# Performance work log

Hardware: AMD Instinct MI355X
Metric: run time of the kernel (lower is better)

The kernel has to match this reference:

```python
import jax, jax.numpy as jnp
import numpy as np

SEQ, BATCH, IN, HID, OUT = 2048, 128, 256, 512, 256


def setup_inputs() -> dict:
    key = jax.random.key(0)
    ks = jax.random.split(key, 7)
    s_ih = 1.0 / np.sqrt(HID)
    return {
        "x": jax.random.normal(ks[0], (SEQ, BATCH, IN), dtype=jnp.float32),
        "W_ih": jax.random.normal(ks[1], (HID, IN), dtype=jnp.float32) * s_ih,
        "W_hh": jax.random.normal(ks[2], (HID, HID), dtype=jnp.float32) * s_ih,
        "b_ih": jax.random.normal(ks[3], (HID,), dtype=jnp.float32) * s_ih,
        "b_hh": jax.random.normal(ks[4], (HID,), dtype=jnp.float32) * s_ih,
        "W_fc": jax.random.normal(ks[5], (OUT, HID), dtype=jnp.float32) * s_ih,
        "b_fc": jax.random.normal(ks[6], (OUT,), dtype=jnp.float32) * s_ih,
    }


def reference(x, W_ih, W_hh, b_ih, b_hh, W_fc, b_fc):
    # Precompute input projections for all timesteps with one big GEMM:
    # [S, B, I] @ [I, H] -> [S, B, H]
    x_proj = jnp.einsum("sbi,hi->sbh", x, W_ih) + b_ih + b_hh

    def step(h, xp):  # h: [B, H], xp: [B, H]
        h_new = jnp.tanh(xp + h @ W_hh.T)
        return h_new, None

    h0 = jnp.zeros((x.shape[1], W_hh.shape[0]), dtype=x.dtype)
    h_last, _ = jax.lax.scan(step, h0, x_proj)
    # fc on last timestep's hidden state -> [B, OUT]
    return h_last @ W_fc.T + b_fc
```

## Files before the change

kernel.cpp:

```cpp
#include <hip/hip_runtime.h>
#include <stdint.h>

#define SEQ   2048
#define BATCH 128
#define DIN   256
#define DH    512
#define DOUT  256

typedef uint16_t u16;
typedef uint32_t u32;
typedef __attribute__((ext_vector_type(8))) short short8;
typedef __attribute__((ext_vector_type(4))) float f32x4;
typedef __attribute__((ext_vector_type(4))) int i32x4;

#define TWO_LOG2E 2.8853900817779268f

__device__ __forceinline__ u16 f2bf(float f) {
    u32 u = __float_as_uint(f);
    u += 0x7fffu + ((u >> 16) & 1u);
    return (u16)(u >> 16);
}
__device__ __forceinline__ float bf2f(u16 h) {
    return __uint_as_float(((u32)h) << 16);
}

__global__ __launch_bounds__(256) void wmax_kernel(const float* __restrict__ W,
                                                   unsigned* __restrict__ wmax) {
    __shared__ float red[256];
    int idx = blockIdx.x * 256 + threadIdx.x;
    float m = 0.f;
#pragma unroll
    for (int j = 0; j < 4; ++j) m = fmaxf(m, fabsf(W[(size_t)idx * 4 + j]));
    red[threadIdx.x] = m;
    __syncthreads();
    for (int s = 128; s > 0; s >>= 1) {
        if (threadIdx.x < s) red[threadIdx.x] = fmaxf(red[threadIdx.x], red[threadIdx.x + s]);
        __syncthreads();
    }
    if (threadIdx.x == 0) atomicMax(wmax, __float_as_uint(red[0]));
}

__global__ __launch_bounds__(256) void pack_whh_i8_kernel(
    const float* __restrict__ W, const unsigned* __restrict__ wmax,
    char* __restrict__ Wq) {
    int idx  = blockIdx.x * 256 + threadIdx.x;
    int lane = idx & 63;
    int n    = (idx >> 6) & 3;
    int kc   = (idx >> 8) & 7;
    int wv   = idx >> 11;
    float s = 127.0f / __uint_as_float(*wmax);
    int col = wv * 64 + n * 16 + (lane & 15);
    int k0  = kc * 64 + (lane >> 4) * 16;
    char q[16];
#pragma unroll
    for (int j = 0; j < 16; ++j)
        q[j] = (char)(int)rintf(W[(size_t)col * DH + k0 + j] * s);
    *reinterpret_cast<i32x4*>(Wq + (size_t)idx * 16) = *reinterpret_cast<i32x4*>(q);
}

__global__ __launch_bounds__(512) void xproj_kernel(
    const float* __restrict__ x, const float* __restrict__ W_ih,
    const float* __restrict__ b_ih, const float* __restrict__ b_hh,
    u16* __restrict__ xp) {
    __shared__ u16 As[128 * 64];
    __shared__ u16 Bs[256 * 64];
    const int tid  = threadIdx.x;
    const int lane = tid & 63;
    const int wid  = tid >> 6;
    const int wm   = wid >> 2;
    const int wn   = wid & 3;
    const int mt   = blockIdx.x;
    const int nt   = blockIdx.y;

    f32x4 acc[4][4];
#pragma unroll
    for (int i = 0; i < 4; ++i)
#pragma unroll
        for (int j = 0; j < 4; ++j) acc[i][j] = (f32x4){0.f, 0.f, 0.f, 0.f};

    for (int kk = 0; kk < DIN; kk += 64) {
        __syncthreads();
        {
            int r = tid >> 2, q = tid & 3;
            const float4* gp = (const float4*)(x + (size_t)(mt * 128 + r) * DIN + kk + q * 16);
            float4 v0 = gp[0], v1 = gp[1], v2 = gp[2], v3 = gp[3];
            short8 h0, h1;
            h0[0]=(short)f2bf(v0.x); h0[1]=(short)f2bf(v0.y); h0[2]=(short)f2bf(v0.z); h0[3]=(short)f2bf(v0.w);
            h0[4]=(short)f2bf(v1.x); h0[5]=(short)f2bf(v1.y); h0[6]=(short)f2bf(v1.z); h0[7]=(short)f2bf(v1.w);
            h1[0]=(short)f2bf(v2.x); h1[1]=(short)f2bf(v2.y); h1[2]=(short)f2bf(v2.z); h1[3]=(short)f2bf(v2.w);
            h1[4]=(short)f2bf(v3.x); h1[5]=(short)f2bf(v3.y); h1[6]=(short)f2bf(v3.z); h1[7]=(short)f2bf(v3.w);
            int base = r * 64, sw = (r & 7) << 3, ke = q * 16;
            *(short8*)&As[base + (ke ^ sw)]       = h0;
            *(short8*)&As[base + ((ke + 8) ^ sw)] = h1;
        }
        {
            int r = tid >> 1, hf = tid & 1;
            const float4* gp = (const float4*)(W_ih + (size_t)(nt * 256 + r) * DIN + kk + hf * 32);
            int base = r * 64, sw = (r & 7) << 3;
#pragma unroll
            for (int cp = 0; cp < 2; ++cp) {
                float4 u0 = gp[cp*4+0], u1 = gp[cp*4+1], u2 = gp[cp*4+2], u3 = gp[cp*4+3];
                short8 t0, t1;
                t0[0]=(short)f2bf(u0.x); t0[1]=(short)f2bf(u0.y); t0[2]=(short)f2bf(u0.z); t0[3]=(short)f2bf(u0.w);
                t0[4]=(short)f2bf(u1.x); t0[5]=(short)f2bf(u1.y); t0[6]=(short)f2bf(u1.z); t0[7]=(short)f2bf(u1.w);
                t1[0]=(short)f2bf(u2.x); t1[1]=(short)f2bf(u2.y); t1[2]=(short)f2bf(u2.z); t1[3]=(short)f2bf(u2.w);
                t1[4]=(short)f2bf(u3.x); t1[5]=(short)f2bf(u3.y); t1[6]=(short)f2bf(u3.z); t1[7]=(short)f2bf(u3.w);
                int ke = hf * 32 + cp * 16;
                *(short8*)&Bs[base + (ke ^ sw)]       = t0;
                *(short8*)&Bs[base + ((ke + 8) ^ sw)] = t1;
            }
        }
        __syncthreads();
#pragma unroll
        for (int kt = 0; kt < 2; ++kt) {
            short8 a[4], b[4];
            int ke = kt * 32 + (lane >> 4) * 8;
#pragma unroll
            for (int mi = 0; mi < 4; ++mi) {
                int rr = wm * 64 + mi * 16 + (lane & 15);
                a[mi] = *(const short8*)&As[rr * 64 + (ke ^ ((rr & 7) << 3))];
            }
#pragma unroll
            for (int ni = 0; ni < 4; ++ni) {
                int rr = wn * 64 + ni * 16 + (lane & 15);
                b[ni] = *(const short8*)&Bs[rr * 64 + (ke ^ ((rr & 7) << 3))];
            }
#pragma unroll
            for (int mi = 0; mi < 4; ++mi)
#pragma unroll
                for (int ni = 0; ni < 4; ++ni)
                    acc[mi][ni] = __builtin_amdgcn_mfma_f32_16x16x32_bf16(b[ni], a[mi], acc[mi][ni], 0, 0, 0);
        }
    }
    const int lq = lane >> 4;
#pragma unroll
    for (int ni = 0; ni < 4; ++ni) {
        int col0 = nt * 256 + wn * 64 + ni * 16 + lq * 4;
        float4 bi = *(const float4*)(b_ih + col0);
        float4 bh = *(const float4*)(b_hh + col0);
        float bb0 = bi.x + bh.x, bb1 = bi.y + bh.y, bb2 = bi.z + bh.z, bb3 = bi.w + bh.w;
#pragma unroll
        for (int mi = 0; mi < 4; ++mi) {
            float v0 = (acc[mi][ni][0] + bb0) * TWO_LOG2E;
            float v1 = (acc[mi][ni][1] + bb1) * TWO_LOG2E;
            float v2 = (acc[mi][ni][2] + bb2) * TWO_LOG2E;
            float v3 = (acc[mi][ni][3] + bb3) * TWO_LOG2E;
            uint2 v;
            v.x = (u32)f2bf(v0) | ((u32)f2bf(v1) << 16);
            v.y = (u32)f2bf(v2) | ((u32)f2bf(v3) << 16);
            int bbk = wm * 4 + mi;
            int cidx = (nt * 4 + wn) * 4 + ni;
            *(uint2*)(xp + ((((size_t)mt * 8 + bbk) * 32 + cidx) * 64 + lane) * 4) = v;
        }
    }
}

__device__ __forceinline__ void rec_epi(
    const i32x4& acc, uint2 xc, float sc2, int t, int row, int colb, int sw,
    char* __restrict__ h_nxt, u16* __restrict__ h_last, int bg) {
    float t0 = fmaf((float)acc[0], sc2, __uint_as_float(xc.x << 16));
    float t1 = fmaf((float)acc[1], sc2, __uint_as_float(xc.x & 0xffff0000u));
    float t2 = fmaf((float)acc[2], sc2, __uint_as_float(xc.y << 16));
    float t3 = fmaf((float)acc[3], sc2, __uint_as_float(xc.y & 0xffff0000u));
    float r0 = __builtin_amdgcn_rcpf(exp2f(t0) + 1.0f);
    float r1 = __builtin_amdgcn_rcpf(exp2f(t1) + 1.0f);
    float r2 = __builtin_amdgcn_rcpf(exp2f(t2) + 1.0f);
    float r3 = __builtin_amdgcn_rcpf(exp2f(t3) + 1.0f);
    if (t == SEQ - 1) {
        float h0 = fmaf(-2.f, r0, 1.f), h1 = fmaf(-2.f, r1, 1.f);
        float h2 = fmaf(-2.f, r2, 1.f), h3 = fmaf(-2.f, r3, 1.f);
        uint2 hv;
        hv.x = (u32)f2bf(h0) | ((u32)f2bf(h1) << 16);
        hv.y = (u32)f2bf(h2) | ((u32)f2bf(h3) << 16);
        *(uint2*)(h_last + (size_t)(bg * 16 + row) * DH + colb) = hv;
    } else {
        u32 b0 = __float_as_uint(fmaf(-254.f, r0, 12583039.f));
        u32 b1 = __float_as_uint(fmaf(-254.f, r1, 12583039.f));
        u32 b2 = __float_as_uint(fmaf(-254.f, r2, 12583039.f));
        u32 b3 = __float_as_uint(fmaf(-254.f, r3, 12583039.f));
        u32 p01 = __builtin_amdgcn_perm(b1, b0, 0x00000400u);
        u32 p23 = __builtin_amdgcn_perm(b3, b2, 0x00000400u);
        u32 pk  = __builtin_amdgcn_perm(p23, p01, 0x05040100u);
        *(u32*)&h_nxt[row * 512 + (colb ^ sw)] = pk;
    }
}

__global__ __launch_bounds__(512) void rnn_rec_kernel(
    const u16* __restrict__ xp, const char* __restrict__ Wq,
    const unsigned* __restrict__ wmax_p, u16* __restrict__ h_last) {
    __shared__ char h_s[2][16 * 512];
    const int tid = threadIdx.x, lane = tid & 63, wv = tid >> 6;
    const int bg = blockIdx.x;
    const int row = lane & 15, lq = lane >> 4;
    const int sw = (row & 7) << 4;
    const float sc2 = __uint_as_float(*wmax_p) * (TWO_LOG2E / (127.f * 127.f));

    i32x4 wrr[8][4];
#pragma unroll
    for (int kc = 0; kc < 8; ++kc)
#pragma unroll
        for (int n = 0; n < 4; ++n) {
            wrr[kc][n] = *(const i32x4*)(Wq + (size_t)((wv * 8 + kc) * 4 + n) * 1024 + lane * 16);
            asm volatile("" : "+v"(wrr[kc][n]));
        }

    *(i32x4*)&h_s[0][tid * 32]      = (i32x4){0, 0, 0, 0};
    *(i32x4*)&h_s[0][tid * 32 + 16] = (i32x4){0, 0, 0, 0};

    const u16* xpp = xp + (((size_t)(bg * 32 + wv * 4) * 64) + lane) * 4;
    uint2 xn[4];
#pragma unroll
    for (int n = 0; n < 4; ++n) xn[n] = *(const uint2*)(xpp + n * 256);
    xpp += 65536;

    __syncthreads();

    for (int t = 0; t < SEQ; ++t) {
        const int cur = t & 1, nxt = cur ^ 1;
        char* h_nxt = h_s[nxt];

        uint2 xc[4];
#pragma unroll
        for (int n = 0; n < 4; ++n) xc[n] = xn[n];
        if (t + 1 < SEQ) {
#pragma unroll
            for (int n = 0; n < 4; ++n) xn[n] = *(const uint2*)(xpp + n * 256);
            xpp += 65536;
        }

        i32x4 a0 = (i32x4){0,0,0,0}, a1 = (i32x4){0,0,0,0};
        __builtin_amdgcn_s_setprio(1);
#pragma unroll
        for (int kc = 0; kc < 8; ++kc) {
            i32x4 hf = *(const i32x4*)&h_s[cur][row * 512 + ((kc * 64 + lq * 16) ^ sw)];
            a0 = __builtin_amdgcn_mfma_i32_16x16x64_i8(wrr[kc][0], hf, a0, 0, 0, 0);
            a1 = __builtin_amdgcn_mfma_i32_16x16x64_i8(wrr[kc][1], hf, a1, 0, 0, 0);
        }
        __builtin_amdgcn_s_setprio(0);
        __builtin_amdgcn_sched_barrier(0);
        rec_epi(a0, xc[0], sc2, t, row, wv * 64 + 0 * 16 + lq * 4, sw, h_nxt, h_last, bg);
        rec_epi(a1, xc[1], sc2, t, row, wv * 64 + 1 * 16 + lq * 4, sw, h_nxt, h_last, bg);
        __builtin_amdgcn_sched_barrier(0);

        i32x4 a2 = (i32x4){0,0,0,0}, a3 = (i32x4){0,0,0,0};
        __builtin_amdgcn_s_setprio(1);
#pragma unroll
        for (int kc = 0; kc < 8; ++kc) {
            i32x4 hf = *(const i32x4*)&h_s[cur][row * 512 + ((kc * 64 + lq * 16) ^ sw)];
            a2 = __builtin_amdgcn_mfma_i32_16x16x64_i8(wrr[kc][2], hf, a2, 0, 0, 0);
            a3 = __builtin_amdgcn_mfma_i32_16x16x64_i8(wrr[kc][3], hf, a3, 0, 0, 0);
        }
        __builtin_amdgcn_s_setprio(0);
        __builtin_amdgcn_sched_barrier(0);
        rec_epi(a2, xc[2], sc2, t, row, wv * 64 + 2 * 16 + lq * 4, sw, h_nxt, h_last, bg);
        rec_epi(a3, xc[3], sc2, t, row, wv * 64 + 3 * 16 + lq * 4, sw, h_nxt, h_last, bg);

        if (t == SEQ - 1) break;
        __syncthreads();
    }
}

__global__ __launch_bounds__(256) void fc_kernel(
    const u16* __restrict__ h_last, const float* __restrict__ W_fc,
    const float* __restrict__ b_fc, float* __restrict__ out) {
    __shared__ float hsh[DH];
    int b = blockIdx.x, o = threadIdx.x;
    for (int i = threadIdx.x; i < DH; i += 256) hsh[i] = bf2f(h_last[(size_t)b * DH + i]);
    __syncthreads();
    const float* w = W_fc + (size_t)o * DH;
    float s = 0.f;
#pragma unroll 8
    for (int k = 0; k < DH; ++k) s += hsh[k] * w[k];
    out[(size_t)b * DOUT + o] = s + b_fc[o];
}

extern "C" void kernel_launch(void* const* d_in, const int* in_sizes, int n_in,
                              void* d_out, int out_size, void* d_ws, size_t ws_size,
                              hipStream_t stream) {
    const float* x    = (const float*)d_in[0];
    const float* W_ih = (const float*)d_in[1];
    const float* W_hh = (const float*)d_in[2];
    const float* b_ih = (const float*)d_in[3];
    const float* b_hh = (const float*)d_in[4];
    const float* W_fc = (const float*)d_in[5];
    const float* b_fc = (const float*)d_in[6];
    float* out = (float*)d_out;

    char* base    = (char*)d_ws;
    u16*  xp      = (u16*)base;
    char* Wq      = base + (size_t)SEQ * BATCH * DH * 2;
    u16*  h_last  = (u16*)(Wq + (size_t)DH * DH);
    unsigned* wmx = (unsigned*)((char*)h_last + (size_t)BATCH * DH * 2);

    hipMemsetAsync(wmx, 0, sizeof(unsigned), stream);
    hipLaunchKernelGGL(wmax_kernel, dim3(256), dim3(256), 0, stream, W_hh, wmx);
    hipLaunchKernelGGL(pack_whh_i8_kernel, dim3(64), dim3(256), 0, stream, W_hh, wmx, Wq);
    hipLaunchKernelGGL(xproj_kernel, dim3(2048, 2), dim3(512), 0, stream, x, W_ih, b_ih, b_hh, xp);
    hipLaunchKernelGGL(rnn_rec_kernel, dim3(8), dim3(512), 0, stream, xp, Wq, wmx, h_last);
    hipLaunchKernelGGL(fc_kernel, dim3(128), dim3(256), 0, stream, h_last, W_fc, b_fc, out);
}
```

Baseline: 3.286 ms.

## Replace per-step block barrier with per-wave LDS flags and rotated K order

Each timestep's __syncthreads is replaced by per-wave progress flags in shared memory. Each wave first consumes the K-chunk of h it produced itself, then spin-waits (with s_sleep) only on the specific wave whose chunk it needs next. The weight registers are reordered to match this rotated K order. The two half-passes with two accumulators each are merged into one pass over K with four accumulators, followed by all four epilogues. The aim is to let waves overlap across timesteps instead of stalling at a full barrier. The cost is spin polling, a reliance on LDS store ordering via lgkmcnt, and a subtle correctness dependence on the double-buffer reuse ordering.

```diff
diff --git a/kernel.cpp b/kernel.cpp
--- a/kernel.cpp
+++ b/kernel.cpp
@@ -189,6 +189,7 @@
     const u16* __restrict__ xp, const char* __restrict__ Wq,
     const unsigned* __restrict__ wmax_p, u16* __restrict__ h_last) {
     __shared__ char h_s[2][16 * 512];
+    __shared__ int hflag[8];
     const int tid = threadIdx.x, lane = tid & 63, wv = tid >> 6;
     const int bg = blockIdx.x;
     const int row = lane & 15, lq = lane >> 4;
@@ -197,15 +198,18 @@
 
     i32x4 wrr[8][4];
 #pragma unroll
-    for (int kc = 0; kc < 8; ++kc)
+    for (int k = 0; k < 8; ++k) {
+        int c = (wv + k) & 7;
 #pragma unroll
         for (int n = 0; n < 4; ++n) {
-            wrr[kc][n] = *(const i32x4*)(Wq + (size_t)((wv * 8 + kc) * 4 + n) * 1024 + lane * 16);
-            asm volatile("" : "+v"(wrr[kc][n]));
-        }
+            wrr[k][n] = *(const i32x4*)(Wq + (size_t)((wv * 8 + c) * 4 + n) * 1024 + lane * 16);
+            asm volatile("" : "+v"(wrr[k][n]));
+        }
+    }
 
     *(i32x4*)&h_s[0][tid * 32]      = (i32x4){0, 0, 0, 0};
     *(i32x4*)&h_s[0][tid * 32 + 16] = (i32x4){0, 0, 0, 0};
+    if (tid < 8) hflag[tid] = 0;
 
     const u16* xpp = xp + (((size_t)(bg * 32 + wv * 4) * 64) + lane) * 4;
     uint2 xn[4];
@@ -228,35 +232,34 @@
             xpp += 65536;
         }
 
-        i32x4 a0 = (i32x4){0,0,0,0}, a1 = (i32x4){0,0,0,0};
-        __builtin_amdgcn_s_setprio(1);
-#pragma unroll
-        for (int kc = 0; kc < 8; ++kc) {
-            i32x4 hf = *(const i32x4*)&h_s[cur][row * 512 + ((kc * 64 + lq * 16) ^ sw)];
-            a0 = __builtin_amdgcn_mfma_i32_16x16x64_i8(wrr[kc][0], hf, a0, 0, 0, 0);
-            a1 = __builtin_amdgcn_mfma_i32_16x16x64_i8(wrr[kc][1], hf, a1, 0, 0, 0);
-        }
-        __builtin_amdgcn_s_setprio(0);
+        i32x4 acc[4];
+#pragma unroll
+        for (int n = 0; n < 4; ++n) acc[n] = (i32x4){0, 0, 0, 0};
+
+#pragma unroll
+        for (int k = 0; k < 8; ++k) {
+            const int c = (wv + k) & 7;
+            if (k) {
+                volatile int* fl = &hflag[c];
+                if (__builtin_expect(*fl < t, 0)) {
+                    do { __builtin_amdgcn_s_sleep(1); } while (*fl < t);
+                }
+                __builtin_amdgcn_sched_barrier(0);
+            }
+            i32x4 hf = *(const i32x4*)&h_s[cur][row * 512 + ((c * 64 + lq * 16) ^ sw)];
+#pragma unroll
+            for (int n = 0; n < 4; ++n)
+                acc[n] = __builtin_amdgcn_mfma_i32_16x16x64_i8(wrr[k][n], hf, acc[n], 0, 0, 0);
+        }
+
+#pragma unroll
+        for (int n = 0; n < 4; ++n)
+            rec_epi(acc[n], xc[n], sc2, t, row, wv * 64 + n * 16 + lq * 4, sw, h_nxt, h_last, bg);
+
+        if (t == SEQ - 1) break;
+        asm volatile("s_waitcnt lgkmcnt(0)" ::: "memory");
+        if (lane == 0) *(volatile int*)&hflag[wv] = t + 1;
         __builtin_amdgcn_sched_barrier(0);
-        rec_epi(a0, xc[0], sc2, t, row, wv * 64 + 0 * 16 + lq * 4, sw, h_nxt, h_last, bg);
-        rec_epi(a1, xc[1], sc2, t, row, wv * 64 + 1 * 16 + lq * 4, sw, h_nxt, h_last, bg);
-        __builtin_amdgcn_sched_barrier(0);
-
-        i32x4 a2 = (i32x4){0,0,0,0}, a3 = (i32x4){0,0,0,0};
-        __builtin_amdgcn_s_setprio(1);
-#pragma unroll
-        for (int kc = 0; kc < 8; ++kc) {
-            i32x4 hf = *(const i32x4*)&h_s[cur][row * 512 + ((kc * 64 + lq * 16) ^ sw)];
-            a2 = __builtin_amdgcn_mfma_i32_16x16x64_i8(wrr[kc][2], hf, a2, 0, 0, 0);
-            a3 = __builtin_amdgcn_mfma_i32_16x16x64_i8(wrr[kc][3], hf, a3, 0, 0, 0);
-        }
-        __builtin_amdgcn_s_setprio(0);
-        __builtin_amdgcn_sched_barrier(0);
-        rec_epi(a2, xc[2], sc2, t, row, wv * 64 + 2 * 16 + lq * 4, sw, h_nxt, h_last, bg);
-        rec_epi(a3, xc[3], sc2, t, row, wv * 64 + 3 * 16 + lq * 4, sw, h_nxt, h_last, bg);
-
-        if (t == SEQ - 1) break;
-        __syncthreads();
     }
 }
 
```

After: 3.882 ms. 1.18x slower.
